# Kernel optimization log

Measured on AMD Instinct MI355X. Metric: run time of the kernel, lower is better.

## Reference

```python
import jax, jax.numpy as jnp
import numpy as np

HIDDEN = 2048
N_HEADS = 16
HEAD_DIM = 128
ROPE_THETA = 10000.0


def setup_inputs() -> dict:
    key = jax.random.key(0)
    k1, k2, k3, k4, k5 = jax.random.split(key, 5)
    B, S = 2, 2048
    return {
        "hidden_states": jax.random.normal(k1, (B, S, HIDDEN), dtype=jnp.float32),
        "position_ids": jnp.arange(S, dtype=jnp.int32)[None, :],  # (1, S)
        "q_kernel": jax.random.normal(k2, (HIDDEN, N_HEADS * HEAD_DIM), dtype=jnp.float32),
        "k_kernel": jax.random.normal(k3, (HIDDEN, N_HEADS * HEAD_DIM), dtype=jnp.float32),
        "v_kernel": jax.random.normal(k4, (HIDDEN, N_HEADS * HEAD_DIM), dtype=jnp.float32),
        "o_kernel": jax.random.normal(k5, (N_HEADS * HEAD_DIM, HIDDEN), dtype=jnp.float32),
    }


def _rotate_half(x):
    half = x.shape[-1] // 2
    return jnp.concatenate([-x[..., half:], x[..., :half]], axis=-1)


def _rope_cos_sin(position_ids):
    # hidden_dim for RoPE = hidden_size // num_heads = HEAD_DIM
    inv_freq = (1.0 / (ROPE_THETA ** (np.arange(0, HEAD_DIM, 2, dtype=np.float32) / HEAD_DIM))).astype(np.float32)
    p32 = position_ids.astype(jnp.float32)[0]  # (S,)
    freqs = jnp.einsum("i,d->id", p32, jnp.asarray(inv_freq))  # (S, Dh/2)
    cos = jnp.concatenate([jnp.cos(freqs), jnp.cos(freqs)], axis=-1)  # (S, Dh)
    sin = jnp.concatenate([jnp.sin(freqs), jnp.sin(freqs)], axis=-1)
    # broadcast to (1, 1, S, Dh) against q/k of shape (B, H, S, Dh)
    return cos[None, None], sin[None, None]


def reference(hidden_states, position_ids, q_kernel, k_kernel, v_kernel, o_kernel):
    B, S, D = hidden_states.shape
    def proj(w):
        return jnp.einsum("bsd,do->bso", hidden_states, w).reshape(B, S, N_HEADS, HEAD_DIM).transpose(0, 2, 1, 3)
    q, k, v = proj(q_kernel), proj(k_kernel), proj(v_kernel)  # (B, H, S, Dh)

    cos, sin = _rope_cos_sin(position_ids)
    q = q * cos + _rotate_half(q) * sin
    k = k * cos + _rotate_half(k) * sin

    scale = 1.0 / jnp.sqrt(jnp.asarray(HEAD_DIM, dtype=q.dtype))
    attn = jnp.einsum("bhqd,bhkd->bhqk", q, k) * scale
    attn = jax.nn.softmax(attn, axis=-1)
    out = jnp.einsum("bhqk,bhkd->bhqd", attn, v)
    out = out.transpose(0, 2, 1, 3).reshape(B, S, N_HEADS * HEAD_DIM)
    return jnp.einsum("bsd,do->bso", out, o_kernel)
```

## Files before the change

kernel.cpp:

```cpp
#include <hip/hip_runtime.h>

typedef unsigned short u16;
typedef __attribute__((ext_vector_type(4))) float f32x4;
typedef __attribute__((ext_vector_type(8))) short short8;

#define MFMA16(a,b,c) __builtin_amdgcn_mfma_f32_16x16x32_bf16((a),(b),(c),0,0,0)

__device__ __forceinline__ u16 f2bf(float f){
  unsigned u = __float_as_uint(f);
  u += 0x7fffu + ((u>>16)&1u);
  return (u16)(u>>16);
}
__device__ __forceinline__ float bf2f(u16 s){ return __uint_as_float(((unsigned)s)<<16); }

__device__ __forceinline__ void glds16(const void* g, void* l){
  __builtin_amdgcn_global_load_lds(
    (const __attribute__((address_space(1))) unsigned int*)g,
    (__attribute__((address_space(3))) unsigned int*)l, 16, 0, 0);
}


__global__ __launch_bounds__(256) void k_split_hidden(const float4* __restrict__ H,
    u16* __restrict__ Hh, u16* __restrict__ Hl){
  int i = blockIdx.x*256 + threadIdx.x;
  float4 v = H[i];
  u16 h0=f2bf(v.x), h1=f2bf(v.y), h2=f2bf(v.z), h3=f2bf(v.w);
  ushort4 hi = make_ushort4(h0,h1,h2,h3);
  ushort4 lo = make_ushort4(f2bf(v.x-bf2f(h0)), f2bf(v.y-bf2f(h1)),
                            f2bf(v.z-bf2f(h2)), f2bf(v.w-bf2f(h3)));
  *(ushort4*)(Hh + (size_t)i*4) = hi;
  *(ushort4*)(Hl + (size_t)i*4) = lo;
}

__global__ __launch_bounds__(256) void k_prep_w1(const float* __restrict__ W,
    u16* __restrict__ hiT, u16* __restrict__ loT, int write_lo){
  __shared__ float tile[64][65];
  int k0 = blockIdx.x*64, n0 = blockIdx.y*64;
  int t = threadIdx.x;
  #pragma unroll 4
  for (int i=0;i<16;i++){
    int idx = t + i*256; int r = idx>>6, c = idx&63;
    tile[r][c] = W[(size_t)(k0+r)*2048 + n0 + c];
  }
  __syncthreads();
  #pragma unroll 4
  for (int i=0;i<16;i++){
    int idx = t + i*256; int r = idx>>6, c = idx&63;
    float v = tile[c][r];
    u16 hi = f2bf(v);
    size_t o = (size_t)(n0+r)*2048 + k0 + c;
    hiT[o] = hi;
    if (write_lo) loT[o] = f2bf(v - bf2f(hi));
  }
}

__global__ __launch_bounds__(256) void k_rope_tab(const int* __restrict__ pos,
    float* __restrict__ ct, float* __restrict__ st){
  int i = blockIdx.x*256 + threadIdx.x;
  int s = i>>6, j = i&63;
  float p = (float)pos[s];
  float inv = exp2f(-(float)j * 0.20762050593046014f);
  float a = p*inv;
  ct[i] = cosf(a); st[i] = sinf(a);
}

__global__ __launch_bounds__(256) void k_gemm_split(
    const u16* __restrict__ Ah, const u16* __restrict__ Al,
    const u16* __restrict__ Bh, const u16* __restrict__ Bl,
    u16* __restrict__ Oh, u16* __restrict__ Ol)
{
  __shared__ __align__(16) u16 lAh[128*32], lAl[128*32], lBh[128*32], lBl[128*32];
  int m0 = blockIdx.x*128, n0 = blockIdx.y*128;
  int tid = threadIdx.x, lane = tid&63, w = tid>>6;
  int wr = w>>1, wc = w&1, g = lane>>4, r = lane&15;
  f32x4 acc[4][4];
  #pragma unroll
  for (int i=0;i<4;i++)
    #pragma unroll
    for (int j=0;j<4;j++)
      #pragma unroll
      for (int e=0;e<4;e++) acc[i][j][e]=0.f;

  for (int k0=0;k0<2048;k0+=32){
    __syncthreads();
    #pragma unroll
    for (int c=0;c<2;c++){
      int off = (w*2+c)*1024 + lane*16;
      int row = off>>6, colb = off&63;
      size_t ga = ((size_t)(m0+row)*2048 + k0)*2 + colb;
      size_t gb = ((size_t)(n0+row)*2048 + k0)*2 + colb;
      int lo = (w*2+c)*1024;
      glds16((const char*)Ah + ga, (char*)lAh + lo);
      glds16((const char*)Bh + gb, (char*)lBh + lo);
      glds16((const char*)Al + ga, (char*)lAl + lo);
      glds16((const char*)Bl + gb, (char*)lBl + lo);
    }
    asm volatile("s_waitcnt vmcnt(0)" ::: "memory");
    __syncthreads();
    short8 ah[4], al[4];
    #pragma unroll
    for (int mi=0;mi<4;mi++){
      int row = wr*64 + mi*16 + r;
      ah[mi] = *(const short8*)((const char*)lAh + row*64 + g*16);
      al[mi] = *(const short8*)((const char*)lAl + row*64 + g*16);
    }
    #pragma unroll
    for (int ni=0;ni<4;ni++){
      int row = wc*64 + ni*16 + r;
      short8 b_h = *(const short8*)((const char*)lBh + row*64 + g*16);
      short8 b_l = *(const short8*)((const char*)lBl + row*64 + g*16);
      #pragma unroll
      for (int mi=0;mi<4;mi++){
        acc[mi][ni] = MFMA16(ah[mi], b_h, acc[mi][ni]);
        acc[mi][ni] = MFMA16(ah[mi], b_l, acc[mi][ni]);
        acc[mi][ni] = MFMA16(al[mi], b_h, acc[mi][ni]);
      }
    }
  }
  #pragma unroll
  for (int mi=0;mi<4;mi++){
    #pragma unroll
    for (int rr=0;rr<4;rr++){
      int m = m0 + wr*64 + mi*16 + g*4 + rr;
      int b = m>>11, s = m&2047;
      #pragma unroll
      for (int ni=0;ni<4;ni++){
        int n = n0 + wc*64 + ni*16 + r;
        int h = n>>7, d = n&127;
        size_t o = (((size_t)((b<<4)+h)*2048 + s)<<7) + d;
        float v = acc[mi][ni][rr];
        u16 hi = f2bf(v);
        Oh[o] = hi;
        Ol[o] = f2bf(v - bf2f(hi));
      }
    }
  }
}

__global__ __launch_bounds__(256) void k_gemm_plain_bf(
    const u16* __restrict__ Ah, const u16* __restrict__ Bh, u16* __restrict__ O)
{
  __shared__ __align__(16) u16 lA[128*32], lB[128*32];
  int m0 = blockIdx.x*128, n0 = blockIdx.y*128;
  int tid = threadIdx.x, lane = tid&63, w = tid>>6;
  int wr = w>>1, wc = w&1, g = lane>>4, r = lane&15;
  f32x4 acc[4][4];
  #pragma unroll
  for (int i=0;i<4;i++)
    #pragma unroll
    for (int j=0;j<4;j++)
      #pragma unroll
      for (int e=0;e<4;e++) acc[i][j][e]=0.f;
  for (int k0=0;k0<2048;k0+=32){
    __syncthreads();
    #pragma unroll
    for (int c=0;c<2;c++){
      int off = (w*2+c)*1024 + lane*16;
      int row = off>>6, colb = off&63;
      size_t ga = ((size_t)(m0+row)*2048 + k0)*2 + colb;
      size_t gb = ((size_t)(n0+row)*2048 + k0)*2 + colb;
      int lo = (w*2+c)*1024;
      glds16((const char*)Ah + ga, (char*)lA + lo);
      glds16((const char*)Bh + gb, (char*)lB + lo);
    }
    asm volatile("s_waitcnt vmcnt(0)" ::: "memory");
    __syncthreads();
    short8 af[4];
    #pragma unroll
    for (int mi=0;mi<4;mi++){
      int row = wr*64 + mi*16 + r;
      af[mi] = *(const short8*)((const char*)lA + row*64 + g*16);
    }
    #pragma unroll
    for (int ni=0;ni<4;ni++){
      int row = wc*64 + ni*16 + r;
      short8 b8 = *(const short8*)((const char*)lB + row*64 + g*16);
      #pragma unroll
      for (int mi=0;mi<4;mi++)
        acc[mi][ni] = MFMA16(af[mi], b8, acc[mi][ni]);
    }
  }
  #pragma unroll
  for (int mi=0;mi<4;mi++){
    #pragma unroll
    for (int rr=0;rr<4;rr++){
      int row = m0 + wr*64 + mi*16 + g*4 + rr;
      #pragma unroll
      for (int ni=0;ni<4;ni++){
        int col = n0 + wc*64 + ni*16 + r;
        O[(size_t)row*2048+col] = f2bf(acc[mi][ni][rr]);
      }
    }
  }
}

__global__ __launch_bounds__(256) void k_rope_ip(u16* __restrict__ Xh, u16* __restrict__ Xl,
    const float* __restrict__ ct, const float* __restrict__ st){
  int i = blockIdx.x*256 + threadIdx.x;
  int row = i>>6, j = i&63;
  int s = row & 2047;
  size_t base = (size_t)row*128;
  float x1 = bf2f(Xh[base+j])    + bf2f(Xl[base+j]);
  float x2 = bf2f(Xh[base+64+j]) + bf2f(Xl[base+64+j]);
  float c = ct[s*64+j], sn = st[s*64+j];
  float o1 = x1*c - x2*sn, o2 = x2*c + x1*sn;
  u16 a1 = f2bf(o1), a2 = f2bf(o2);
  Xh[base+j]    = a1; Xl[base+j]    = f2bf(o1 - bf2f(a1));
  Xh[base+64+j] = a2; Xl[base+64+j] = f2bf(o2 - bf2f(a2));
}

__global__ __launch_bounds__(256) void k_vt(const u16* __restrict__ Vb, u16* __restrict__ VT){
  __shared__ u16 tile[128][129];
  int bh = blockIdx.y, b = bh>>4, h = bh&15;
  int s0 = blockIdx.x*128;
  int t = threadIdx.x;
  #pragma unroll 4
  for (int i=0;i<16;i++){
    int idx = i*1024 + t*4; int srow = idx>>7, c = idx&127;
    const u16* gp = Vb + ((size_t)(b*2048+s0+srow))*2048 + h*128 + c;
    ushort4 v = *(const ushort4*)gp;
    tile[srow][c]=v.x; tile[srow][c+1]=v.y; tile[srow][c+2]=v.z; tile[srow][c+3]=v.w;
  }
  __syncthreads();
  #pragma unroll 4
  for (int i=0;i<16;i++){
    int idx = i*1024 + t*4; int drow = idx>>7, s = idx&127;
    ushort4 v = make_ushort4(tile[s][drow], tile[s+1][drow], tile[s+2][drow], tile[s+3][drow]);
    *(ushort4*)(VT + ((size_t)(bh*128+drow))*2048 + s0 + s) = v;
  }
}

__global__ __launch_bounds__(256) void k_attn(
  const u16* __restrict__ Qh, const u16* __restrict__ Ql,
  const u16* __restrict__ Kh, const u16* __restrict__ Kl,
  const u16* __restrict__ VT, u16* __restrict__ AO)
{
  __shared__ __align__(16) u16 lKh[64*128], lKl[64*128], lVT[128*64];
  __shared__ __align__(16) u16 lP[4*16*72];
  int bh = blockIdx.y, q0 = blockIdx.x*64;
  int tid = threadIdx.x, lane = tid&63, w = tid>>6;
  int g = lane>>4, r = lane&15;
  const float SC = 0.12751878329866064f;
  short8 qh[4], ql[4];
  {
    size_t qb = ((size_t)bh*2048 + q0 + w*16 + r)*128;
    #pragma unroll
    for (int ks=0;ks<4;ks++){
      qh[ks] = *(const short8*)(Qh + qb + ks*32 + g*8);
      ql[ks] = *(const short8*)(Ql + qb + ks*32 + g*8);
    }
  }
  f32x4 o[8];
  #pragma unroll
  for (int i=0;i<8;i++)
    #pragma unroll
    for (int e=0;e<4;e++) o[i][e]=0.f;
  float mrow[4] = {-3.0e38f,-3.0e38f,-3.0e38f,-3.0e38f};
  float lrow[4] = {0.f,0.f,0.f,0.f};
  size_t kb = (size_t)bh*2048*128;
  size_t vbase = (size_t)bh*128*2048;

  for (int kv0=0;kv0<2048;kv0+=64){
    __syncthreads();
    #pragma unroll
    for (int c=0;c<4;c++){
      int off = (w*4+c)*1024 + lane*16;
      int lo = (w*4+c)*1024;
      int row = off>>8, ch = (off>>4)&15;
      int chs = (ch&8)|((ch^row)&7);
      size_t gk = (kb + (size_t)(kv0+row)*128)*2 + chs*16;
      glds16((const char*)Kh + gk, (char*)lKh + lo);
      glds16((const char*)Kl + gk, (char*)lKl + lo);
      int rowd = off>>7, ch2 = (off>>4)&7;
      int chs2 = (ch2^rowd)&7;
      size_t gv = (vbase + (size_t)rowd*2048 + kv0)*2 + chs2*16;
      glds16((const char*)VT + gv, (char*)lVT + lo);
    }
    asm volatile("s_waitcnt vmcnt(0)" ::: "memory");
    __syncthreads();

    f32x4 s4[4];
    #pragma unroll
    for (int i=0;i<4;i++)
      #pragma unroll
      for (int e=0;e<4;e++) s4[i][e]=0.f;
    #pragma unroll
    for (int ks=0;ks<4;ks++){
      #pragma unroll
      for (int ni=0;ni<4;ni++){
        int kvr = ni*16 + r;
        int ch = ks*4 + g;
        int chs = (ch&8)|((ch^kvr)&7);
        short8 kh8 = *(const short8*)((const char*)lKh + kvr*256 + chs*16);
        short8 kl8 = *(const short8*)((const char*)lKl + kvr*256 + chs*16);
        s4[ni] = MFMA16(qh[ks], kh8, s4[ni]);
        s4[ni] = MFMA16(qh[ks], kl8, s4[ni]);
        s4[ni] = MFMA16(ql[ks], kh8, s4[ni]);
      }
    }
    float pm[4], f[4], rs[4];
    #pragma unroll
    for (int rr=0;rr<4;rr++){
      float m = fmaxf(fmaxf(s4[0][rr], s4[1][rr]), fmaxf(s4[2][rr], s4[3][rr]));
      m = fmaxf(m, __shfl_xor(m,1));
      m = fmaxf(m, __shfl_xor(m,2));
      m = fmaxf(m, __shfl_xor(m,4));
      m = fmaxf(m, __shfl_xor(m,8));
      pm[rr]=m;
    }
    #pragma unroll
    for (int rr=0;rr<4;rr++){
      float mn = fmaxf(mrow[rr], pm[rr]);
      f[rr] = exp2f((mrow[rr]-mn)*SC);
      mrow[rr]=mn; lrow[rr]*=f[rr];
    }
    #pragma unroll
    for (int nd=0;nd<8;nd++)
      #pragma unroll
      for (int rr=0;rr<4;rr++) o[nd][rr] *= f[rr];
    #pragma unroll
    for (int rr=0;rr<4;rr++) rs[rr]=0.f;
    #pragma unroll
    for (int ni=0;ni<4;ni++){
      #pragma unroll
      for (int rr=0;rr<4;rr++){
        float p = exp2f((s4[ni][rr]-mrow[rr])*SC);
        rs[rr] += p;
        lP[w*1152 + (g*4+rr)*72 + ni*16 + r] = f2bf(p);
      }
    }
    #pragma unroll
    for (int rr=0;rr<4;rr++){
      float x = rs[rr];
      x += __shfl_xor(x,1); x += __shfl_xor(x,2);
      x += __shfl_xor(x,4); x += __shfl_xor(x,8);
      lrow[rr] += x;
    }
    #pragma unroll
    for (int ks2=0;ks2<2;ks2++){
      short8 pa = *(const short8*)((const char*)lP + w*2304 + r*144 + ks2*64 + g*16);
      #pragma unroll
      for (int nd=0;nd<8;nd++){
        int dr = nd*16 + r;
        int chs = ((ks2*4+g)^dr)&7;
        short8 v8 = *(const short8*)((const char*)lVT + dr*128 + chs*16);
        o[nd] = MFMA16(pa, v8, o[nd]);
      }
    }
  }
  int b = bh>>4, h = bh&15;
  #pragma unroll
  for (int rr=0;rr<4;rr++){
    float inv = 1.0f/lrow[rr];
    int row = b*2048 + q0 + w*16 + g*4 + rr;
    #pragma unroll
    for (int nd=0;nd<8;nd++){
      int col = h*128 + nd*16 + r;
      AO[(size_t)row*2048 + col] = f2bf(o[nd][rr]*inv);
    }
  }
}

__global__ __launch_bounds__(256) void k_gemm_out(
    const u16* __restrict__ A, const u16* __restrict__ Bt, float* __restrict__ C)
{
  __shared__ __align__(16) u16 lA[128*32], lB[128*32];
  int m0 = blockIdx.x*128, n0 = blockIdx.y*128;
  int tid = threadIdx.x, lane = tid&63, w = tid>>6;
  int wr = w>>1, wc = w&1, g = lane>>4, r = lane&15;
  f32x4 acc[4][4];
  #pragma unroll
  for (int i=0;i<4;i++)
    #pragma unroll
    for (int j=0;j<4;j++)
      #pragma unroll
      for (int e=0;e<4;e++) acc[i][j][e]=0.f;
  for (int k0=0;k0<2048;k0+=32){
    __syncthreads();
    #pragma unroll
    for (int c=0;c<2;c++){
      int off = (w*2+c)*1024 + lane*16;
      int row = off>>6, colb = off&63;
      size_t ga = ((size_t)(m0+row)*2048 + k0)*2 + colb;
      size_t gb = ((size_t)(n0+row)*2048 + k0)*2 + colb;
      int lo = (w*2+c)*1024;
      glds16((const char*)A + ga, (char*)lA + lo);
      glds16((const char*)Bt + gb, (char*)lB + lo);
    }
    asm volatile("s_waitcnt vmcnt(0)" ::: "memory");
    __syncthreads();
    short8 af[4];
    #pragma unroll
    for (int mi=0;mi<4;mi++){
      int row = wr*64 + mi*16 + r;
      af[mi] = *(const short8*)((const char*)lA + row*64 + g*16);
    }
    #pragma unroll
    for (int ni=0;ni<4;ni++){
      int row = wc*64 + ni*16 + r;
      short8 b8 = *(const short8*)((const char*)lB + row*64 + g*16);
      #pragma unroll
      for (int mi=0;mi<4;mi++)
        acc[mi][ni] = MFMA16(af[mi], b8, acc[mi][ni]);
    }
  }
  #pragma unroll
  for (int mi=0;mi<4;mi++){
    #pragma unroll
    for (int rr=0;rr<4;rr++){
      int row = m0 + wr*64 + mi*16 + g*4 + rr;
      #pragma unroll
      for (int ni=0;ni<4;ni++){
        int col = n0 + wc*64 + ni*16 + r;
        C[(size_t)row*2048+col] = acc[mi][ni][rr];
      }
    }
  }
}

extern "C" void kernel_launch(void* const* d_in, const int* in_sizes, int n_in,
                              void* d_out, int out_size, void* d_ws, size_t ws_size,
                              hipStream_t stream){
  const float* Hsrc = (const float*)d_in[0];
  const int*   pids = (const int*)d_in[1];
  const float* Wq   = (const float*)d_in[2];
  const float* Wk   = (const float*)d_in[3];
  const float* Wv   = (const float*)d_in[4];
  const float* Wo   = (const float*)d_in[5];
  float* out = (float*)d_out;

  char* p = (char*)d_ws;
  u16* Hh  = (u16*)(p);
  u16* Hl  = (u16*)(p +  16777216);
  u16* Wbh = (u16*)(p +  33554432);
  u16* Wbl = (u16*)(p +  41943040);
  u16* Qsh = (u16*)(p +  50331648);
  u16* Qsl = (u16*)(p +  67108864);
  u16* Ksh = (u16*)(p +  83886080);
  u16* Ksl = (u16*)(p + 100663296);
  u16* Vb  = (u16*)(p + 117440512);
  float* ct = (float*)(p + 134217728);
  float* st = (float*)(p + 134742016);
  u16* VT = Hh;
  u16* AO = Hl;

  k_split_hidden<<<8192,256,0,stream>>>((const float4*)Hsrc, Hh, Hl);
  k_rope_tab<<<512,256,0,stream>>>(pids, ct, st);

  k_prep_w1<<<dim3(32,32),256,0,stream>>>(Wq, Wbh, Wbl, 1);
  k_gemm_split<<<dim3(32,16),256,0,stream>>>(Hh, Hl, Wbh, Wbl, Qsh, Qsl);
  k_prep_w1<<<dim3(32,32),256,0,stream>>>(Wk, Wbh, Wbl, 1);
  k_gemm_split<<<dim3(32,16),256,0,stream>>>(Hh, Hl, Wbh, Wbl, Ksh, Ksl);
  k_prep_w1<<<dim3(32,32),256,0,stream>>>(Wv, Wbh, Wbl, 0);
  k_gemm_plain_bf<<<dim3(32,16),256,0,stream>>>(Hh, Wbh, Vb);

  k_vt<<<dim3(16,32),256,0,stream>>>(Vb, VT);
  k_rope_ip<<<16384,256,0,stream>>>(Qsh, Qsl, ct, st);
  k_rope_ip<<<16384,256,0,stream>>>(Ksh, Ksl, ct, st);
  k_prep_w1<<<dim3(32,32),256,0,stream>>>(Wo, Wbh, Wbl, 0);

  k_attn<<<dim3(32,32),256,0,stream>>>(Qsh, Qsl, Ksh, Ksl, VT, AO);
  k_gemm_out<<<dim3(32,16),256,0,stream>>>(AO, Wbh, out);
}
```

Measured before the change: 701.1 us.

## Fuse RoPE into QK projection, write V transposed, batch weight prep, retile attention

Batches the Q/K/V weight conversions into one launch and runs the Q and K projections as a single launch over a z dimension. Each block now covers one full head, so RoPE is applied in the GEMM epilogue and the separate RoPE and V-transpose kernels go away. The V projection writes its output already transposed. The attention kernel moves to 32-wide KV tiles, skips the rescale when no row max changes, defers the row-sum reduction to the end, and raises wave priority around the MFMA blocks. Together these cut launches and intermediate memory round trips, at the cost of twice as many KV-loop iterations and changed tile shapes.

```diff
diff --git a/kernel.cpp b/kernel.cpp
--- a/kernel.cpp
+++ b/kernel.cpp
@@ -32,8 +32,12 @@
   *(ushort4*)(Hl + (size_t)i*4) = lo;
 }
 
-__global__ __launch_bounds__(256) void k_prep_w1(const float* __restrict__ W,
-    u16* __restrict__ hiT, u16* __restrict__ loT, int write_lo){
+__global__ __launch_bounds__(256) void k_prep_w3(
+    const float* __restrict__ Wq, const float* __restrict__ Wk, const float* __restrict__ Wv,
+    u16* __restrict__ Wqh, u16* __restrict__ Wql,
+    u16* __restrict__ Wkh, u16* __restrict__ Wkl, u16* __restrict__ Wvh){
+  int z = blockIdx.z;
+  const float* W = (z==0)?Wq:((z==1)?Wk:Wv);
   __shared__ float tile[64][65];
   int k0 = blockIdx.x*64, n0 = blockIdx.y*64;
   int t = threadIdx.x;
@@ -49,8 +53,27 @@
     float v = tile[c][r];
     u16 hi = f2bf(v);
     size_t o = (size_t)(n0+r)*2048 + k0 + c;
-    hiT[o] = hi;
-    if (write_lo) loT[o] = f2bf(v - bf2f(hi));
+    if (z==0){ Wqh[o]=hi; Wql[o]=f2bf(v - bf2f(hi)); }
+    else if (z==1){ Wkh[o]=hi; Wkl[o]=f2bf(v - bf2f(hi)); }
+    else { Wvh[o]=hi; }
+  }
+}
+
+__global__ __launch_bounds__(256) void k_prep_w1(const float* __restrict__ W,
+    u16* __restrict__ hiT){
+  __shared__ float tile[64][65];
+  int k0 = blockIdx.x*64, n0 = blockIdx.y*64;
+  int t = threadIdx.x;
+  #pragma unroll 4
+  for (int i=0;i<16;i++){
+    int idx = t + i*256; int r = idx>>6, c = idx&63;
+    tile[r][c] = W[(size_t)(k0+r)*2048 + n0 + c];
+  }
+  __syncthreads();
+  #pragma unroll 4
+  for (int i=0;i<16;i++){
+    int idx = t + i*256; int r = idx>>6, c = idx&63;
+    hiT[(size_t)(n0+r)*2048 + k0 + c] = f2bf(tile[c][r]);
   }
 }
 
@@ -64,20 +87,28 @@
   ct[i] = cosf(a); st[i] = sinf(a);
 }
 
-__global__ __launch_bounds__(256) void k_gemm_split(
-    const u16* __restrict__ Ah, const u16* __restrict__ Al,
-    const u16* __restrict__ Bh, const u16* __restrict__ Bl,
-    u16* __restrict__ Oh, u16* __restrict__ Ol)
+__global__ __launch_bounds__(256) void k_gemm_qk(
+    const u16* __restrict__ Hh, const u16* __restrict__ Hl,
+    const u16* __restrict__ Wqh, const u16* __restrict__ Wql,
+    const u16* __restrict__ Wkh, const u16* __restrict__ Wkl,
+    const float* __restrict__ ct, const float* __restrict__ st,
+    u16* __restrict__ Qh, u16* __restrict__ Ql,
+    u16* __restrict__ Kh, u16* __restrict__ Kl)
 {
+  int z = blockIdx.z;
+  const u16* Bh = z ? Wkh : Wqh;
+  const u16* Bl = z ? Wkl : Wql;
+  u16* Oh = z ? Kh : Qh;
+  u16* Ol = z ? Kl : Ql;
   __shared__ __align__(16) u16 lAh[128*32], lAl[128*32], lBh[128*32], lBl[128*32];
-  int m0 = blockIdx.x*128, n0 = blockIdx.y*128;
+  int m0 = blockIdx.x*128, h = blockIdx.y;
   int tid = threadIdx.x, lane = tid&63, w = tid>>6;
-  int wr = w>>1, wc = w&1, g = lane>>4, r = lane&15;
-  f32x4 acc[4][4];
-  #pragma unroll
-  for (int i=0;i<4;i++)
-    #pragma unroll
-    for (int j=0;j<4;j++)
+  int g = lane>>4, r = lane&15;
+  f32x4 acc[2][8];
+  #pragma unroll
+  for (int i=0;i<2;i++)
+    #pragma unroll
+    for (int j=0;j<8;j++)
       #pragma unroll
       for (int e=0;e<4;e++) acc[i][j][e]=0.f;
 
@@ -88,67 +119,69 @@
       int off = (w*2+c)*1024 + lane*16;
       int row = off>>6, colb = off&63;
       size_t ga = ((size_t)(m0+row)*2048 + k0)*2 + colb;
-      size_t gb = ((size_t)(n0+row)*2048 + k0)*2 + colb;
+      size_t gb = ((size_t)(h*128+row)*2048 + k0)*2 + colb;
       int lo = (w*2+c)*1024;
-      glds16((const char*)Ah + ga, (char*)lAh + lo);
+      glds16((const char*)Hh + ga, (char*)lAh + lo);
+      glds16((const char*)Hl + ga, (char*)lAl + lo);
       glds16((const char*)Bh + gb, (char*)lBh + lo);
-      glds16((const char*)Al + ga, (char*)lAl + lo);
       glds16((const char*)Bl + gb, (char*)lBl + lo);
     }
     asm volatile("s_waitcnt vmcnt(0)" ::: "memory");
     __syncthreads();
-    short8 ah[4], al[4];
-    #pragma unroll
-    for (int mi=0;mi<4;mi++){
-      int row = wr*64 + mi*16 + r;
-      ah[mi] = *(const short8*)((const char*)lAh + row*64 + g*16);
-      al[mi] = *(const short8*)((const char*)lAl + row*64 + g*16);
-    }
-    #pragma unroll
-    for (int ni=0;ni<4;ni++){
-      int row = wc*64 + ni*16 + r;
+    short8 a_h[2], a_l[2];
+    #pragma unroll
+    for (int mi=0;mi<2;mi++){
+      int row = w*32 + mi*16 + r;
+      a_h[mi] = *(const short8*)((const char*)lAh + row*64 + g*16);
+      a_l[mi] = *(const short8*)((const char*)lAl + row*64 + g*16);
+    }
+    #pragma unroll
+    for (int ni=0;ni<8;ni++){
+      int row = ni*16 + r;
       short8 b_h = *(const short8*)((const char*)lBh + row*64 + g*16);
       short8 b_l = *(const short8*)((const char*)lBl + row*64 + g*16);
       #pragma unroll
-      for (int mi=0;mi<4;mi++){
-        acc[mi][ni] = MFMA16(ah[mi], b_h, acc[mi][ni]);
-        acc[mi][ni] = MFMA16(ah[mi], b_l, acc[mi][ni]);
-        acc[mi][ni] = MFMA16(al[mi], b_h, acc[mi][ni]);
-      }
-    }
-  }
-  #pragma unroll
-  for (int mi=0;mi<4;mi++){
+      for (int mi=0;mi<2;mi++){
+        acc[mi][ni] = MFMA16(a_h[mi], b_h, acc[mi][ni]);
+        acc[mi][ni] = MFMA16(a_h[mi], b_l, acc[mi][ni]);
+        acc[mi][ni] = MFMA16(a_l[mi], b_h, acc[mi][ni]);
+      }
+    }
+  }
+  int b = m0>>11;
+  int bh = b*16 + h;
+  #pragma unroll
+  for (int mi=0;mi<2;mi++){
     #pragma unroll
     for (int rr=0;rr<4;rr++){
-      int m = m0 + wr*64 + mi*16 + g*4 + rr;
-      int b = m>>11, s = m&2047;
+      int s = (m0&2047) + w*32 + mi*16 + g*4 + rr;
+      size_t rowbase = ((size_t)bh*2048 + s)*128;
       #pragma unroll
       for (int ni=0;ni<4;ni++){
-        int n = n0 + wc*64 + ni*16 + r;
-        int h = n>>7, d = n&127;
-        size_t o = (((size_t)((b<<4)+h)*2048 + s)<<7) + d;
-        float v = acc[mi][ni][rr];
-        u16 hi = f2bf(v);
-        Oh[o] = hi;
-        Ol[o] = f2bf(v - bf2f(hi));
-      }
-    }
-  }
-}
-
-__global__ __launch_bounds__(256) void k_gemm_plain_bf(
-    const u16* __restrict__ Ah, const u16* __restrict__ Bh, u16* __restrict__ O)
+        int j = ni*16 + r;
+        float c = ct[s*64 + j], sn = st[s*64 + j];
+        float x1 = acc[mi][ni][rr], x2 = acc[mi][ni+4][rr];
+        float o1 = x1*c - x2*sn;
+        float o2 = x2*c + x1*sn;
+        u16 h1 = f2bf(o1); Oh[rowbase + j] = h1;      Ol[rowbase + j]      = f2bf(o1 - bf2f(h1));
+        u16 h2 = f2bf(o2); Oh[rowbase + 64 + j] = h2; Ol[rowbase + 64 + j] = f2bf(o2 - bf2f(h2));
+      }
+    }
+  }
+}
+
+__global__ __launch_bounds__(256) void k_gemm_v(
+    const u16* __restrict__ Hh, const u16* __restrict__ Wvh, u16* __restrict__ VT)
 {
   __shared__ __align__(16) u16 lA[128*32], lB[128*32];
-  int m0 = blockIdx.x*128, n0 = blockIdx.y*128;
+  int m0 = blockIdx.x*128, h = blockIdx.y;
   int tid = threadIdx.x, lane = tid&63, w = tid>>6;
-  int wr = w>>1, wc = w&1, g = lane>>4, r = lane&15;
-  f32x4 acc[4][4];
-  #pragma unroll
-  for (int i=0;i<4;i++)
-    #pragma unroll
-    for (int j=0;j<4;j++)
+  int g = lane>>4, r = lane&15;
+  f32x4 acc[2][8];
+  #pragma unroll
+  for (int i=0;i<2;i++)
+    #pragma unroll
+    for (int j=0;j<8;j++)
       #pragma unroll
       for (int e=0;e<4;e++) acc[i][j][e]=0.f;
   for (int k0=0;k0<2048;k0+=32){
@@ -158,75 +191,40 @@
       int off = (w*2+c)*1024 + lane*16;
       int row = off>>6, colb = off&63;
       size_t ga = ((size_t)(m0+row)*2048 + k0)*2 + colb;
-      size_t gb = ((size_t)(n0+row)*2048 + k0)*2 + colb;
+      size_t gb = ((size_t)(h*128+row)*2048 + k0)*2 + colb;
       int lo = (w*2+c)*1024;
-      glds16((const char*)Ah + ga, (char*)lA + lo);
-      glds16((const char*)Bh + gb, (char*)lB + lo);
+      glds16((const char*)Hh + ga, (char*)lA + lo);
+      glds16((const char*)Wvh + gb, (char*)lB + lo);
     }
     asm volatile("s_waitcnt vmcnt(0)" ::: "memory");
     __syncthreads();
-    short8 af[4];
-    #pragma unroll
-    for (int mi=0;mi<4;mi++){
-      int row = wr*64 + mi*16 + r;
-      af[mi] = *(const short8*)((const char*)lA + row*64 + g*16);
-    }
-    #pragma unroll
-    for (int ni=0;ni<4;ni++){
-      int row = wc*64 + ni*16 + r;
-      short8 b8 = *(const short8*)((const char*)lB + row*64 + g*16);
-      #pragma unroll
-      for (int mi=0;mi<4;mi++)
-        acc[mi][ni] = MFMA16(af[mi], b8, acc[mi][ni]);
-    }
-  }
-  #pragma unroll
-  for (int mi=0;mi<4;mi++){
-    #pragma unroll
-    for (int rr=0;rr<4;rr++){
-      int row = m0 + wr*64 + mi*16 + g*4 + rr;
-      #pragma unroll
-      for (int ni=0;ni<4;ni++){
-        int col = n0 + wc*64 + ni*16 + r;
-        O[(size_t)row*2048+col] = f2bf(acc[mi][ni][rr]);
-      }
-    }
-  }
-}
-
-__global__ __launch_bounds__(256) void k_rope_ip(u16* __restrict__ Xh, u16* __restrict__ Xl,
-    const float* __restrict__ ct, const float* __restrict__ st){
-  int i = blockIdx.x*256 + threadIdx.x;
-  int row = i>>6, j = i&63;
-  int s = row & 2047;
-  size_t base = (size_t)row*128;
-  float x1 = bf2f(Xh[base+j])    + bf2f(Xl[base+j]);
-  float x2 = bf2f(Xh[base+64+j]) + bf2f(Xl[base+64+j]);
-  float c = ct[s*64+j], sn = st[s*64+j];
-  float o1 = x1*c - x2*sn, o2 = x2*c + x1*sn;
-  u16 a1 = f2bf(o1), a2 = f2bf(o2);
-  Xh[base+j]    = a1; Xl[base+j]    = f2bf(o1 - bf2f(a1));
-  Xh[base+64+j] = a2; Xl[base+64+j] = f2bf(o2 - bf2f(a2));
-}
-
-__global__ __launch_bounds__(256) void k_vt(const u16* __restrict__ Vb, u16* __restrict__ VT){
-  __shared__ u16 tile[128][129];
-  int bh = blockIdx.y, b = bh>>4, h = bh&15;
-  int s0 = blockIdx.x*128;
-  int t = threadIdx.x;
-  #pragma unroll 4
-  for (int i=0;i<16;i++){
-    int idx = i*1024 + t*4; int srow = idx>>7, c = idx&127;
-    const u16* gp = Vb + ((size_t)(b*2048+s0+srow))*2048 + h*128 + c;
-    ushort4 v = *(const ushort4*)gp;
-    tile[srow][c]=v.x; tile[srow][c+1]=v.y; tile[srow][c+2]=v.z; tile[srow][c+3]=v.w;
-  }
-  __syncthreads();
-  #pragma unroll 4
-  for (int i=0;i<16;i++){
-    int idx = i*1024 + t*4; int drow = idx>>7, s = idx&127;
-    ushort4 v = make_ushort4(tile[s][drow], tile[s+1][drow], tile[s+2][drow], tile[s+3][drow]);
-    *(ushort4*)(VT + ((size_t)(bh*128+drow))*2048 + s0 + s) = v;
+    short8 a_h[2];
+    #pragma unroll
+    for (int mi=0;mi<2;mi++){
+      int row = w*32 + mi*16 + r;
+      a_h[mi] = *(const short8*)((const char*)lA + row*64 + g*16);
+    }
+    #pragma unroll
+    for (int ni=0;ni<8;ni++){
+      int row = ni*16 + r;
+      short8 b_h = *(const short8*)((const char*)lB + row*64 + g*16);
+      #pragma unroll
+      for (int mi=0;mi<2;mi++)
+        acc[mi][ni] = MFMA16(a_h[mi], b_h, acc[mi][ni]);
+    }
+  }
+  int b = m0>>11;
+  int bh = b*16 + h;
+  #pragma unroll
+  for (int mi=0;mi<2;mi++){
+    int sb = (m0&2047) + w*32 + mi*16 + g*4;
+    #pragma unroll
+    for (int ni=0;ni<8;ni++){
+      int d = ni*16 + r;
+      ushort4 vv = make_ushort4(f2bf(acc[mi][ni][0]), f2bf(acc[mi][ni][1]),
+                                f2bf(acc[mi][ni][2]), f2bf(acc[mi][ni][3]));
+      *(ushort4*)(VT + ((size_t)(bh*128 + d))*2048 + sb) = vv;
+    }
   }
 }
 
@@ -235,8 +233,8 @@
   const u16* __restrict__ Kh, const u16* __restrict__ Kl,
   const u16* __restrict__ VT, u16* __restrict__ AO)
 {
-  __shared__ __align__(16) u16 lKh[64*128], lKl[64*128], lVT[128*64];
-  __shared__ __align__(16) u16 lP[4*16*72];
+  __shared__ __align__(16) u16 lKh[32*128], lKl[32*128], lVT[128*32];
+  __shared__ __align__(16) u16 lP[4*16*40];
   int bh = blockIdx.y, q0 = blockIdx.x*64;
   int tid = threadIdx.x, lane = tid&63, w = tid>>6;
   int g = lane>>4, r = lane&15;
@@ -250,103 +248,108 @@
       ql[ks] = *(const short8*)(Ql + qb + ks*32 + g*8);
     }
   }
+  int koff[4];
+  #pragma unroll
+  for (int ks=0;ks<4;ks++){
+    int ch = ks*4 + g;
+    koff[ks] = r*256 + (((ch&8) | ((ch^r)&7))<<4);
+  }
   f32x4 o[8];
   #pragma unroll
   for (int i=0;i<8;i++)
     #pragma unroll
     for (int e=0;e<4;e++) o[i][e]=0.f;
   float mrow[4] = {-3.0e38f,-3.0e38f,-3.0e38f,-3.0e38f};
-  float lrow[4] = {0.f,0.f,0.f,0.f};
+  float lrowl[4] = {0.f,0.f,0.f,0.f};
   size_t kb = (size_t)bh*2048*128;
   size_t vbase = (size_t)bh*128*2048;
 
-  for (int kv0=0;kv0<2048;kv0+=64){
-    __syncthreads();
-    #pragma unroll
-    for (int c=0;c<4;c++){
-      int off = (w*4+c)*1024 + lane*16;
-      int lo = (w*4+c)*1024;
-      int row = off>>8, ch = (off>>4)&15;
-      int chs = (ch&8)|((ch^row)&7);
-      size_t gk = (kb + (size_t)(kv0+row)*128)*2 + chs*16;
+  for (int kv0=0;kv0<2048;kv0+=32){
+    __syncthreads();
+    #pragma unroll
+    for (int c=0;c<2;c++){
+      int off = (w*2+c)*1024 + lane*16;
+      int lo = (w*2+c)*1024;
+      int krow = off>>8, ch = (off>>4)&15;
+      int chs = (ch&8)|((ch^krow)&7);
+      size_t gk = (kb + (size_t)(kv0+krow)*128)*2 + chs*16;
       glds16((const char*)Kh + gk, (char*)lKh + lo);
       glds16((const char*)Kl + gk, (char*)lKl + lo);
-      int rowd = off>>7, ch2 = (off>>4)&7;
-      int chs2 = (ch2^rowd)&7;
-      size_t gv = (vbase + (size_t)rowd*2048 + kv0)*2 + chs2*16;
+      int vrow = off>>6, sch = (off>>4)&3;
+      size_t gv = (vbase + (size_t)vrow*2048 + kv0 + sch*8)*2;
       glds16((const char*)VT + gv, (char*)lVT + lo);
     }
     asm volatile("s_waitcnt vmcnt(0)" ::: "memory");
     __syncthreads();
 
-    f32x4 s4[4];
-    #pragma unroll
-    for (int i=0;i<4;i++)
+    f32x4 s4[2];
+    #pragma unroll
+    for (int i=0;i<2;i++)
       #pragma unroll
       for (int e=0;e<4;e++) s4[i][e]=0.f;
+    __builtin_amdgcn_s_setprio(1);
     #pragma unroll
     for (int ks=0;ks<4;ks++){
       #pragma unroll
-      for (int ni=0;ni<4;ni++){
-        int kvr = ni*16 + r;
-        int ch = ks*4 + g;
-        int chs = (ch&8)|((ch^kvr)&7);
-        short8 kh8 = *(const short8*)((const char*)lKh + kvr*256 + chs*16);
-        short8 kl8 = *(const short8*)((const char*)lKl + kvr*256 + chs*16);
+      for (int ni=0;ni<2;ni++){
+        int a = ni*4096 + koff[ks];
+        short8 kh8 = *(const short8*)((const char*)lKh + a);
+        short8 kl8 = *(const short8*)((const char*)lKl + a);
         s4[ni] = MFMA16(qh[ks], kh8, s4[ni]);
         s4[ni] = MFMA16(qh[ks], kl8, s4[ni]);
         s4[ni] = MFMA16(ql[ks], kh8, s4[ni]);
       }
     }
-    float pm[4], f[4], rs[4];
+    __builtin_amdgcn_s_setprio(0);
+    float pm[4];
     #pragma unroll
     for (int rr=0;rr<4;rr++){
-      float m = fmaxf(fmaxf(s4[0][rr], s4[1][rr]), fmaxf(s4[2][rr], s4[3][rr]));
+      float m = fmaxf(s4[0][rr], s4[1][rr]);
       m = fmaxf(m, __shfl_xor(m,1));
       m = fmaxf(m, __shfl_xor(m,2));
       m = fmaxf(m, __shfl_xor(m,4));
       m = fmaxf(m, __shfl_xor(m,8));
       pm[rr]=m;
     }
-    #pragma unroll
-    for (int rr=0;rr<4;rr++){
-      float mn = fmaxf(mrow[rr], pm[rr]);
-      f[rr] = exp2f((mrow[rr]-mn)*SC);
-      mrow[rr]=mn; lrow[rr]*=f[rr];
-    }
-    #pragma unroll
-    for (int nd=0;nd<8;nd++)
-      #pragma unroll
-      for (int rr=0;rr<4;rr++) o[nd][rr] *= f[rr];
-    #pragma unroll
-    for (int rr=0;rr<4;rr++) rs[rr]=0.f;
-    #pragma unroll
-    for (int ni=0;ni<4;ni++){
+    bool anynew = (pm[0]>mrow[0])|(pm[1]>mrow[1])|(pm[2]>mrow[2])|(pm[3]>mrow[3]);
+    if (__any(anynew)){
+      float f[4];
+      #pragma unroll
+      for (int rr=0;rr<4;rr++){
+        float mn = fmaxf(mrow[rr], pm[rr]);
+        f[rr] = exp2f((mrow[rr]-mn)*SC);
+        mrow[rr]=mn; lrowl[rr]*=f[rr];
+      }
+      #pragma unroll
+      for (int nd=0;nd<8;nd++)
+        #pragma unroll
+        for (int rr=0;rr<4;rr++) o[nd][rr] *= f[rr];
+    }
+    #pragma unroll
+    for (int ni=0;ni<2;ni++){
       #pragma unroll
       for (int rr=0;rr<4;rr++){
         float p = exp2f((s4[ni][rr]-mrow[rr])*SC);
-        rs[rr] += p;
-        lP[w*1152 + (g*4+rr)*72 + ni*16 + r] = f2bf(p);
-      }
-    }
-    #pragma unroll
-    for (int rr=0;rr<4;rr++){
-      float x = rs[rr];
-      x += __shfl_xor(x,1); x += __shfl_xor(x,2);
-      x += __shfl_xor(x,4); x += __shfl_xor(x,8);
-      lrow[rr] += x;
-    }
-    #pragma unroll
-    for (int ks2=0;ks2<2;ks2++){
-      short8 pa = *(const short8*)((const char*)lP + w*2304 + r*144 + ks2*64 + g*16);
-      #pragma unroll
-      for (int nd=0;nd<8;nd++){
-        int dr = nd*16 + r;
-        int chs = ((ks2*4+g)^dr)&7;
-        short8 v8 = *(const short8*)((const char*)lVT + dr*128 + chs*16);
-        o[nd] = MFMA16(pa, v8, o[nd]);
-      }
-    }
+        lrowl[rr] += p;
+        lP[w*640 + (g*4+rr)*40 + ni*16 + r] = f2bf(p);
+      }
+    }
+    short8 pa = *(const short8*)((const char*)lP + w*1280 + r*80 + g*16);
+    __builtin_amdgcn_s_setprio(1);
+    #pragma unroll
+    for (int nd=0;nd<8;nd++){
+      short8 v8 = *(const short8*)((const char*)lVT + (nd*16+r)*64 + g*16);
+      o[nd] = MFMA16(pa, v8, o[nd]);
+    }
+    __builtin_amdgcn_s_setprio(0);
+  }
+  float lrow[4];
+  #pragma unroll
+  for (int rr=0;rr<4;rr++){
+    float x = lrowl[rr];
+    x += __shfl_xor(x,1); x += __shfl_xor(x,2);
+    x += __shfl_xor(x,4); x += __shfl_xor(x,8);
+    lrow[rr] = x;
   }
   int b = bh>>4, h = bh&15;
   #pragma unroll
@@ -432,33 +435,27 @@
   char* p = (char*)d_ws;
   u16* Hh  = (u16*)(p);
   u16* Hl  = (u16*)(p +  16777216);
-  u16* Wbh = (u16*)(p +  33554432);
-  u16* Wbl = (u16*)(p +  41943040);
-  u16* Qsh = (u16*)(p +  50331648);
-  u16* Qsl = (u16*)(p +  67108864);
-  u16* Ksh = (u16*)(p +  83886080);
-  u16* Ksl = (u16*)(p + 100663296);
-  u16* Vb  = (u16*)(p + 117440512);
-  float* ct = (float*)(p + 134217728);
-  float* st = (float*)(p + 134742016);
-  u16* VT = Hh;
-  u16* AO = Hl;
+  u16* Wqh = (u16*)(p +  33554432);
+  u16* Wql = (u16*)(p +  41943040);
+  u16* Wkh = (u16*)(p +  50331648);
+  u16* Wkl = (u16*)(p +  58720256);
+  u16* Wvh = (u16*)(p +  67108864);
+  u16* Qsh = (u16*)(p +  75497472);
+  u16* Qsl = (u16*)(p +  92274688);
+  u16* Ksh = (u16*)(p + 109051904);
+  u16* Ksl = (u16*)(p + 125829120);
+  float* ct = (float*)(p + 142606336);
+  float* st = (float*)(p + 143130624);
+  u16* VT  = Hl;
+  u16* AO  = Hh;
+  u16* Woh = Wqh;
 
   k_split_hidden<<<8192,256,0,stream>>>((const float4*)Hsrc, Hh, Hl);
   k_rope_tab<<<512,256,0,stream>>>(pids, ct, st);
-
-  k_prep_w1<<<dim3(32,32),256,0,stream>>>(Wq, Wbh, Wbl, 1);
-  k_gemm_split<<<dim3(32,16),256,0,stream>>>(Hh, Hl, Wbh, Wbl, Qsh, Qsl);
-  k_prep_w1<<<dim3(32,32),256,0,stream>>>(Wk, Wbh, Wbl, 1);
-  k_gemm_split<<<dim3(32,16),256,0,stream>>>(Hh, Hl, Wbh, Wbl, Ksh, Ksl);
-  k_prep_w1<<<dim3(32,32),256,0,stream>>>(Wv, Wbh, Wbl, 0);
-  k_gemm_plain_bf<<<dim3(32,16),256,0,stream>>>(Hh, Wbh, Vb);
-
-  k_vt<<<dim3(16,32),256,0,stream>>>(Vb, VT);
-  k_rope_ip<<<16384,256,0,stream>>>(Qsh, Qsl, ct, st);
-  k_rope_ip<<<16384,256,0,stream>>>(Ksh, Ksl, ct, st);
-  k_prep_w1<<<dim3(32,32),256,0,stream>>>(Wo, Wbh, Wbl, 0);
-
-  k_attn<<<dim3(32,32),256,0,stream>>>(Qsh, Qsl, Ksh, Ksl, VT, AO);
-  k_gemm_out<<<dim3(32,16),256,0,stream>>>(AO, Wbh, out);
-}
+  k_prep_w3<<<dim3(32,32,3),256,0,stream>>>(Wq,Wk,Wv,Wqh,Wql,Wkh,Wkl,Wvh);
+  k_gemm_qk<<<dim3(32,16,2),256,0,stream>>>(Hh,Hl,Wqh,Wql,Wkh,Wkl,ct,st,Qsh,Qsl,Ksh,Ksl);
+  k_prep_w1<<<dim3(32,32),256,0,stream>>>(Wo, Woh);
+  k_gemm_v<<<dim3(32,16),256,0,stream>>>(Hh, Wvh, VT);
+  k_attn<<<dim3(32,32),256,0,stream>>>(Qsh,Qsl,Ksh,Ksl,VT,AO);
+  k_gemm_out<<<dim3(32,16),256,0,stream>>>(AO, Woh, out);
+}
```

Measured after the change: 722.1 us. +3.0%, slower.
